# Performance work log

Hardware: AMD Instinct MI355X
Metric: run time of the kernel (lower is better)

The kernel has to match this reference:

```python
import math
import jax, jax.numpy as jnp
import numpy as np

C = 64
GRID = 2

def _conv1x1(x, W, b):
    # 1x1 conv == channel-mixing matmul: [B,C,H,W] x [O,C] -> [B,O,H,W]
    return jnp.einsum('bchw,oc->bohw', x, W) + b[None, :, None, None]

def setup_inputs() -> dict:
    key = jax.random.key(0)
    ks = jax.random.split(key, 11)
    s = 1.0 / math.sqrt(C)
    def w(k):
        return jax.random.normal(k, (C, C), dtype=jnp.float32) * s
    def bias(k):
        return jax.random.normal(k, (C,), dtype=jnp.float32) * 0.02
    return {
        'x': jax.random.normal(ks[0], (2, C, 128, 128), dtype=jnp.float32),
        'Wq': w(ks[1]), 'bq': bias(ks[2]),
        'Wk': w(ks[3]), 'bk': bias(ks[4]),
        'Wa': w(ks[5]), 'ba': bias(ks[6]),
        'Wb': w(ks[7]), 'bb': bias(ks[8]),
        'Wo': w(ks[9]), 'bo': bias(ks[10]),
    }

def reference(x, Wq, bq, Wk, bk, Wa, ba, Wb, bb, Wo, bo):
    B, c, H, W = x.shape
    g = GRID
    rh, rw = H // g, W // g  # H,W chosen divisible by grid -> no reflect pad
    N = rh * rw
    R = g * g

    q = _conv1x1(x, Wq, bq)
    k = _conv1x1(x, Wk, bk)
    a = _conv1x1(x, Wa, ba)
    bt = _conv1x1(x, Wb, bb)

    def regionize(t):
        # [B,C,H,W] -> [B, R, C, N] with N = rh*rw row-major per region
        return t.reshape(B, c, g, rh, g, rw).transpose(0, 2, 4, 1, 3, 5).reshape(B, R, c, N)

    qr, kr, ar, br = regionize(q), regionize(k), regionize(a), regionize(bt)

    # attn[b,r,n,m] = softmax_m( q^T k / sqrt(C) )
    attn = jax.nn.softmax(jnp.einsum('brcn,brcm->brnm', qr, kr) / math.sqrt(c), axis=-1)

    # out_r = alpha @ attn + beta @ attn^T
    out = (jnp.einsum('brcj,brjm->brcm', ar, attn)
           + jnp.einsum('brcj,brmj->brcm', br, attn))

    # [B,R,C,N] -> [B,C,H,W]
    out = out.reshape(B, g, g, c, rh, rw).transpose(0, 3, 1, 4, 2, 5).reshape(B, c, H, W)
    return _conv1x1(out, Wo, bo)
```

## Files before the change

kernel.cpp:

```cpp
#include <hip/hip_runtime.h>


typedef __attribute__((ext_vector_type(8)))  short bf16x8;
typedef __attribute__((ext_vector_type(16))) float f32x16;

#define MFMA32(a, b, c) __builtin_amdgcn_mfma_f32_32x32x16_bf16(a, b, c, 0, 0, 0)

constexpr int REG_ELEMS = 4096 * 64;
constexpr size_t QP_OFF    = 0;
constexpr size_t KP_OFF    = 4u  << 20;
constexpr size_t ATL_OFF   = 8u  << 20;
constexpr size_t BTL_OFF   = 12u << 20;
constexpr size_t OUTP_OFF  = 16u << 20;
constexpr size_t LNV_OFF   = 20u << 20;
constexpr size_t LPART_OFF = (20u << 20) + (128u << 10);

constexpr float QSCALE = 0.18033688011112042f;

__device__ __forceinline__ short f2bf(float f) {
    union { float f; unsigned u; } v; v.f = f;
    unsigned r = v.u + 0x7fffu + ((v.u >> 16) & 1u);
    return (short)(r >> 16);
}
__device__ __forceinline__ float bf2f(short s) {
    union { unsigned u; float f; } v; v.u = ((unsigned)(unsigned short)s) << 16;
    return v.f;
}
__device__ __forceinline__ unsigned fbits(float f) {
    union { float f; unsigned u; } v; v.f = f; return v.u;
}
__device__ __forceinline__ unsigned pack_trunc(float e0, float e1) {
    return __builtin_amdgcn_perm(fbits(e1), fbits(e0), 0x07060302u);
}
__device__ __forceinline__ f32x16 zero16() {
    f32x16 z;
    #pragma unroll
    for (int i = 0; i < 16; ++i) z[i] = 0.f;
    return z;
}
__device__ __forceinline__ float fexp2(float x) {
#if __has_builtin(__builtin_amdgcn_exp2f)
    return __builtin_amdgcn_exp2f(x);
#else
    return exp2f(x);
#endif
}
__device__ __forceinline__ void permswap32(unsigned& a, unsigned& b, bool hi) {
#if __has_builtin(__builtin_amdgcn_permlane32_swap)
    auto r = __builtin_amdgcn_permlane32_swap(a, b, false, false);
    a = r[0]; b = r[1];
#elif __has_builtin(__builtin_amdgcn_permlane32_swap_b32)
    auto r = __builtin_amdgcn_permlane32_swap_b32(a, b, false, false);
    a = r[0]; b = r[1];
#else
    unsigned ax = (unsigned)__shfl_xor((int)a, 32);
    unsigned bx = (unsigned)__shfl_xor((int)b, 32);
    unsigned na = hi ? bx : a;
    unsigned nb = hi ? b  : ax;
    a = na; b = nb;
#endif
}

typedef __attribute__((address_space(1))) const unsigned char as1_t;
typedef __attribute__((address_space(3))) unsigned char as3_t;
__device__ __forceinline__ void stage16(const void* g, void* l) {
    __builtin_amdgcn_global_load_lds((as1_t*)g, (as3_t*)l, 16, 0, 0);
}

__global__ __launch_bounds__(256) void k_conv_in(
    const float* __restrict__ x,
    const float* __restrict__ Wq, const float* __restrict__ bq,
    const float* __restrict__ Wk, const float* __restrict__ bk,
    const float* __restrict__ Wa, const float* __restrict__ ba,
    const float* __restrict__ Wb, const float* __restrict__ bb,
    char* __restrict__ ws)
{
    const int tid  = threadIdx.x;
    const int blk  = blockIdx.x;
    const int wseg = blk & 1;
    const int h    = (blk >> 1) & 127;
    const int b    = blk >> 8;
    const int br   = b * 4 + (h >> 6) * 2 + wseg;
    const int n0   = (h & 63) * 64;

    __shared__ float xs[64][68];
    __shared__ short trans[2][64][72];

    const float* xp = x + ((size_t)b * 64 * 16384) + (size_t)h * 128 + wseg * 64;
    #pragma unroll
    for (int r = 0; r < 4; ++r) {
        int idx = r * 256 + tid;
        int c   = idx >> 4;
        int w4  = (idx & 15) << 2;
        *(float4*)&xs[c][w4] = *(const float4*)(xp + (size_t)c * 16384 + w4);
    }
    __syncthreads();

    const int lane = tid & 63;
    const int wid  = tid >> 6;
    const int col  = lane & 31;
    const int l5   = lane >> 5;
    const int pH   = wid & 1;
    const int oH   = wid >> 1;
    const int px   = pH * 32 + col;
    const int oc   = oH * 32 + col;

    bf16x8 xhi[4], xlo[4];
    #pragma unroll
    for (int s = 0; s < 4; ++s) {
        union { bf16x8 v; short sh[8]; } uh, ul;
        #pragma unroll
        for (int e = 0; e < 8; ++e) {
            float xv = xs[s * 16 + l5 * 8 + e][px];
            short hh = f2bf(xv);
            uh.sh[e] = hh;
            ul.sh[e] = f2bf(xv - bf2f(hh));
        }
        xhi[s] = uh.v; xlo[s] = ul.v;
    }

    #pragma unroll
    for (int mat = 0; mat < 4; ++mat) {
        const float* Wsel = (mat == 0) ? Wq : (mat == 1) ? Wk : (mat == 2) ? Wa : Wb;
        const float* bsel = (mat == 0) ? bq : (mat == 1) ? bk : (mat == 2) ? ba : bb;

        bf16x8 whi[4], wlo[4];
        const float* wrow = Wsel + (size_t)oc * 64;
        #pragma unroll
        for (int s = 0; s < 4; ++s) {
            float4 f0 = *(const float4*)(wrow + s * 16 + l5 * 8);
            float4 f1 = *(const float4*)(wrow + s * 16 + l5 * 8 + 4);
            float wf[8] = { f0.x, f0.y, f0.z, f0.w, f1.x, f1.y, f1.z, f1.w };
            union { bf16x8 v; short sh[8]; } uh, ul;
            #pragma unroll
            for (int e = 0; e < 8; ++e) {
                short hh = f2bf(wf[e]);
                uh.sh[e] = hh;
                ul.sh[e] = f2bf(wf[e] - bf2f(hh));
            }
            whi[s] = uh.v; wlo[s] = ul.v;
        }

        f32x16 d = zero16();
        #pragma unroll
        for (int s = 0; s < 4; ++s) {
            d = MFMA32(xhi[s], whi[s], d);
            d = MFMA32(xhi[s], wlo[s], d);
            d = MFMA32(xlo[s], whi[s], d);
        }

        const float bias = bsel[oc];
        if (mat < 2) {
            const float sc = (mat == 0) ? QSCALE : 1.0f;
            #pragma unroll
            for (int r = 0; r < 16; ++r) {
                int pxl = pH * 32 + (r & 3) + 8 * (r >> 2) + 4 * l5;
                trans[mat][pxl][oc] = f2bf((d[r] + bias) * sc);
            }
        } else {
            short* base = (short*)(ws + (mat == 2 ? ATL_OFF : BTL_OFF))
                          + (size_t)br * REG_ELEMS;
            const int sw   = (oc >> 1) & 3;
            const int tile = (n0 >> 5) + pH;
            #pragma unroll
            for (int q = 0; q < 4; ++q) {
                short tmp4[4];
                #pragma unroll
                for (int rr = 0; rr < 4; ++rr) tmp4[rr] = f2bf(d[4 * q + rr] + bias);
                int segp = q ^ sw;
                short* p = base + (size_t)tile * 2048 + oc * 32 + segp * 8 + 4 * l5;
                *(uint2*)p = *(uint2*)tmp4;
            }
        }
    }
    __syncthreads();

    #pragma unroll
    for (int rep = 0; rep < 4; ++rep) {
        int idx  = rep * 256 + tid;
        int mat2 = idx >> 9;
        int row  = (idx >> 3) & 63;
        int seg  = idx & 7;
        short* dst = (short*)(ws + (mat2 ? KP_OFF : QP_OFF))
                     + (size_t)br * REG_ELEMS + (size_t)(n0 + row) * 64
                     + (seg ^ (row & 7)) * 8;
        *(uint4*)dst = *(uint4*)&trans[mat2][row][seg * 8];
    }
}

__global__ __launch_bounds__(256, 2) void k_stats(char* __restrict__ ws)
{
    const int tid  = threadIdx.x;
    const int br   = blockIdx.x & 7;
    const int nt   = (blockIdx.x >> 3) & 63;
    const int ms   = blockIdx.x >> 9;
    const int lane = tid & 63;
    const int w    = tid >> 6;
    const int wn   = w & 1;
    const int wi   = w >> 1;
    const int col  = lane & 31;
    const int l5   = lane >> 5;

    const short* Qb  = (const short*)(ws + QP_OFF) + (size_t)br * REG_ELEMS;
    const char*  Kbb = ws + KP_OFF + (size_t)br * REG_ELEMS * 2
                       + (size_t)ms * 262144;

    __shared__ __align__(16) char smem[16896];

    const int nrow = nt * 64 + wn * 32 + col;
    bf16x8 afr[4];
    #pragma unroll
    for (int s = 0; s < 4; ++s)
        afr[s] = *(const bf16x8*)(Qb + (size_t)nrow * 64 + (((2*s+l5) ^ (col & 7)) * 8));

    float sm[16];
    #pragma unroll
    for (int r = 0; r < 16; ++r) sm[r] = 0.f;

    {
        const char* g = Kbb + (size_t)w * 2048 + lane * 16;
        char* l = smem + w * 2048;
        stage16(g, l); stage16(g + 1024, l + 1024);
    }

    #pragma unroll 2
    for (int slab = 0; slab < 32; ++slab) {
        __syncthreads();
        if (slab + 1 < 32) {
            const char* g = Kbb + (size_t)(slab + 1) * 8192 + w * 2048 + lane * 16;
            char* l = smem + ((slab + 1) & 1) * 8192 + w * 2048;
            stage16(g, l); stage16(g + 1024, l + 1024);
        }
        const short* Ks = (const short*)(smem + (slab & 1) * 8192);
        f32x16 d = zero16();
        #pragma unroll
        for (int s = 0; s < 4; ++s) {
            bf16x8 bf = *(const bf16x8*)(Ks + (wi * 32 + col) * 64
                                         + ((2*s+l5) ^ (col & 7)) * 8);
            d = MFMA32(afr[s], bf, d);
        }
        #pragma unroll
        for (int r = 0; r < 16; ++r) sm[r] += fexp2(d[r]);
    }

    #pragma unroll
    for (int off = 1; off < 32; off <<= 1)
        #pragma unroll
        for (int r = 0; r < 16; ++r) sm[r] += __shfl_xor(sm[r], off);

    __syncthreads();
    float* Lred = (float*)(smem + 16384);
    if (col == 0) {
        #pragma unroll
        for (int r = 0; r < 16; ++r)
            Lred[w * 32 + ((r & 3) + 8 * (r >> 2) + 4 * l5)] = sm[r];
    }
    __syncthreads();
    if (tid < 64) {
        int wn2 = tid >> 5, nl = tid & 31;
        float L = Lred[wn2 * 32 + nl] + Lred[(wn2 + 2) * 32 + nl];
        ((float*)(ws + LPART_OFF))[(size_t)ms * 32768 + (size_t)br * 4096
                                   + nt * 64 + tid] = L;
    }
}

__global__ __launch_bounds__(256) void k_ascale(char* __restrict__ ws)
{
    const int tid = threadIdx.x;
    const int br  = blockIdx.x & 7;
    const int nt  = blockIdx.x >> 3;

    __shared__ float Larr[64];

    if (tid < 64) {
        const float* Lp = (const float*)(ws + LPART_OFF);
        const size_t idx = (size_t)br * 4096 + nt * 64 + tid;
        float li = 1.0f / (Lp[idx] + Lp[32768 + idx]);
        Larr[tid] = li;
        ((float*)(ws + LNV_OFF))[idx] = li;
    }
    __syncthreads();

    short* Ab = (short*)(ws + ATL_OFF) + (size_t)br * REG_ELEMS + (size_t)nt * 4096;
    #pragma unroll
    for (int rep = 0; rep < 2; ++rep) {
        int id = rep * 256 + tid;
        int t = id >> 8, c = (id >> 2) & 63, s = id & 3;
        int sg = s ^ ((c >> 1) & 3);
        int jl = t * 32 + sg * 8;
        short* p = Ab + (size_t)t * 2048 + c * 32 + s * 8;
        uint4 v = *(uint4*)p;
        short* sp = (short*)&v;
        short o[8];
        #pragma unroll
        for (int e = 0; e < 8; ++e) o[e] = f2bf(bf2f(sp[e]) * Larr[jl + e]);
        *(uint4*)p = *(uint4*)o;
    }
}

__global__ __launch_bounds__(256, 2) void k_attn(char* __restrict__ ws)
{
    const int tid  = threadIdx.x;
    const int br   = blockIdx.x & 7;
    const int mt   = blockIdx.x >> 3;
    const int lane = tid & 63;
    const int w    = tid >> 6;
    const int wm   = w & 1;
    const int wj   = w >> 1;
    const int col  = lane & 31;
    const int l5   = lane >> 5;
    const bool hi  = (l5 != 0);

    const char* Qbb = ws + QP_OFF  + (size_t)br * REG_ELEMS * 2;
    const char* Kbb = ws + KP_OFF  + (size_t)br * REG_ELEMS * 2;
    const char* Abb = ws + ATL_OFF + (size_t)br * REG_ELEMS * 2;
    const char* Bbb = ws + BTL_OFF + (size_t)br * REG_ELEMS * 2;
    const float* Lnv = (const float*)(ws + LNV_OFF) + (size_t)br * 4096;
    short* OutPb    = (short*)(ws + OUTP_OFF) + (size_t)br * REG_ELEMS;

    __shared__ __align__(16) char smem[32768];

    const int mrow = mt * 64 + wm * 32 + col;
    const short* msrc = (const short*)(wj == 0 ? Kbb : Qbb) + (size_t)mrow * 64;
    bf16x8 mf[4];
    #pragma unroll
    for (int s = 0; s < 4; ++s)
        mf[s] = *(const bf16x8*)(msrc + ((2*s+l5) ^ (col & 7)) * 8);

    f32x16 accL = zero16(), accH = zero16();

    const char* gsb = (w == 0) ? Qbb : (w == 1) ? Kbb : (w == 2) ? Abb : Bbb;

    {
        const char* g = gsb + lane * 16;
        char* l = smem + w * 4096 + lane * 16;
        #pragma unroll
        for (int i = 0; i < 4; ++i) stage16(g + i * 1024, l + i * 1024);
    }

    #pragma unroll 2
    for (int slab = 0; slab < 128; ++slab) {
        __syncthreads();
        if (slab + 1 < 128) {
            const char* g = gsb + (size_t)(slab + 1) * 4096 + lane * 16;
            char* l = smem + ((slab + 1) & 1) * 16384 + w * 4096 + lane * 16;
            #pragma unroll
            for (int i = 0; i < 4; ++i) stage16(g + i * 1024, l + i * 1024);
        }
        const char* sb = smem + (slab & 1) * 16384;
        const short* js = (const short*)(sb + (wj == 0 ? 0 : 4096));
        const short* ts = (const short*)(sb + (wj == 0 ? 8192 : 12288));

        f32x16 d = zero16();
        #pragma unroll
        for (int s = 0; s < 4; ++s) {
            bf16x8 a = *(const bf16x8*)(js + col * 64 + ((2*s+l5) ^ (col & 7)) * 8);
            d = MFMA32(a, mf[s], d);
        }

        unsigned Wp[8];
        #pragma unroll
        for (int q = 0; q < 4; ++q) {
            Wp[2*q]   = pack_trunc(fexp2(d[4*q]),   fexp2(d[4*q+1]));
            Wp[2*q+1] = pack_trunc(fexp2(d[4*q+2]), fexp2(d[4*q+3]));
        }

        #pragma unroll
        for (int k16 = 0; k16 < 2; ++k16) {
            unsigned u0 = Wp[4*k16+0], u1 = Wp[4*k16+1];
            unsigned u2 = Wp[4*k16+2], u3 = Wp[4*k16+3];
            permswap32(u0, u2, hi);
            permswap32(u1, u3, hi);
            union { uint4 u; bf16x8 v; } fr;
            fr.u.x = u0; fr.u.y = u1; fr.u.z = u2; fr.u.w = u3;

            const int swz = ((2*k16 + l5) ^ ((col >> 1) & 3)) * 8;
            bf16x8 bL = *(const bf16x8*)(ts + col * 32 + swz);
            bf16x8 bH = *(const bf16x8*)(ts + (col + 32) * 32 + swz);
            accL = MFMA32(fr.v, bL, accL);
            accH = MFMA32(fr.v, bH, accH);
        }
    }

    __syncthreads();
    float* red = (float*)smem;
    if (wj == 0) {
        #pragma unroll
        for (int r = 0; r < 16; ++r) {
            int ml = wm * 32 + (r & 3) + 8 * (r >> 2) + 4 * l5;
            red[ml * 68 + col]      = accL[r];
            red[ml * 68 + 32 + col] = accH[r];
        }
    }
    __syncthreads();
    if (wj == 1) {
        #pragma unroll
        for (int r = 0; r < 16; ++r) {
            int ml = wm * 32 + (r & 3) + 8 * (r >> 2) + 4 * l5;
            float li = Lnv[mt * 64 + ml];
            red[ml * 68 + col]      += li * accL[r];
            red[ml * 68 + 32 + col] += li * accH[r];
        }
    }
    __syncthreads();
    {
        const int m  = tid >> 2;
        const int c0 = (tid & 3) * 16;
        const float* rp = red + m * 68 + c0;
        uint4 p0, p1;
        p0.x = pack_trunc(rp[0],  rp[1]);  p0.y = pack_trunc(rp[2],  rp[3]);
        p0.z = pack_trunc(rp[4],  rp[5]);  p0.w = pack_trunc(rp[6],  rp[7]);
        p1.x = pack_trunc(rp[8],  rp[9]);  p1.y = pack_trunc(rp[10], rp[11]);
        p1.z = pack_trunc(rp[12], rp[13]); p1.w = pack_trunc(rp[14], rp[15]);
        short* orow = OutPb + (size_t)(mt * 64 + m) * 64 + c0;
        *(uint4*)orow       = p0;
        *(uint4*)(orow + 8) = p1;
    }
}

__global__ __launch_bounds__(256) void k_conv_out(
    const char* __restrict__ ws,
    const float* __restrict__ Wo, const float* __restrict__ bo,
    float* __restrict__ out)
{
    const int tid  = threadIdx.x;
    const int lane = tid & 63;
    const int sub  = tid >> 6;
    const int blk  = blockIdx.x;
    const int br   = blk & 7;
    const int nt   = (blk >> 3) * 4 + sub;
    const int col  = lane & 31;
    const int l5   = lane >> 5;

    const short* OutPb = (const short*)(ws + OUTP_OFF) + (size_t)br * REG_ELEMS;

    bf16x8 afr[4];
    const short* arow = OutPb + (size_t)(nt * 32 + col) * 64 + l5 * 8;
    #pragma unroll
    for (int s = 0; s < 4; ++s) afr[s] = *(const bf16x8*)(arow + s * 16);

    bf16x8 bw[2][4];
    #pragma unroll
    for (int oh = 0; oh < 2; ++oh) {
        const float* wrow = Wo + (size_t)(oh * 32 + col) * 64 + l5 * 8;
        #pragma unroll
        for (int s = 0; s < 4; ++s) {
            float4 f0 = *(const float4*)(wrow + s * 16);
            float4 f1 = *(const float4*)(wrow + s * 16 + 4);
            union { bf16x8 v; short sh[8]; } u;
            u.sh[0] = f2bf(f0.x); u.sh[1] = f2bf(f0.y);
            u.sh[2] = f2bf(f0.z); u.sh[3] = f2bf(f0.w);
            u.sh[4] = f2bf(f1.x); u.sh[5] = f2bf(f1.y);
            u.sh[6] = f2bf(f1.z); u.sh[7] = f2bf(f1.w);
            bw[oh][s] = u.v;
        }
    }

    f32x16 d0 = zero16(), d1 = zero16();
    #pragma unroll
    for (int s = 0; s < 4; ++s) {
        d0 = MFMA32(afr[s], bw[0][s], d0);
        d1 = MFMA32(afr[s], bw[1][s], d1);
    }

    const int b  = br >> 2;
    const int gi = (br >> 1) & 1;
    const int gj = br & 1;

    #pragma unroll
    for (int oh = 0; oh < 2; ++oh) {
        const int oc = oh * 32 + col;
        const float bias = bo[oc];
        const f32x16& d = oh ? d1 : d0;
        #pragma unroll
        for (int q = 0; q < 4; ++q) {
            int nloc = 8 * q + 4 * l5;
            int nreg = nt * 32 + nloc;
            int wp   = nreg & 63;
            int ip   = nreg >> 6;
            float4 v = make_float4(d[4*q+0] + bias, d[4*q+1] + bias,
                                   d[4*q+2] + bias, d[4*q+3] + bias);
            float* op = out + ((size_t)(b * 64 + oc)) * 16384
                        + (size_t)(gi * 64 + ip) * 128 + gj * 64 + wp;
            *(float4*)op = v;
        }
    }
}

extern "C" void kernel_launch(void* const* d_in, const int* in_sizes, int n_in,
                              void* d_out, int out_size, void* d_ws, size_t ws_size,
                              hipStream_t stream)
{
    const float* x  = (const float*)d_in[0];
    const float* Wq = (const float*)d_in[1];
    const float* bq = (const float*)d_in[2];
    const float* Wk = (const float*)d_in[3];
    const float* bk = (const float*)d_in[4];
    const float* Wa = (const float*)d_in[5];
    const float* ba = (const float*)d_in[6];
    const float* Wb = (const float*)d_in[7];
    const float* bb = (const float*)d_in[8];
    const float* Wo = (const float*)d_in[9];
    const float* bo = (const float*)d_in[10];
    char* ws   = (char*)d_ws;
    float* out = (float*)d_out;

    hipLaunchKernelGGL(k_conv_in,  dim3(512),  dim3(256), 0, stream,
                       x, Wq, bq, Wk, bk, Wa, ba, Wb, bb, ws);
    hipLaunchKernelGGL(k_stats,    dim3(1024), dim3(256), 0, stream, ws);
    hipLaunchKernelGGL(k_ascale,   dim3(512),  dim3(256), 0, stream, ws);
    hipLaunchKernelGGL(k_attn,     dim3(512),  dim3(256), 0, stream, ws);
    hipLaunchKernelGGL(k_conv_out, dim3(256),  dim3(256), 0, stream,
                       ws, Wo, bo, out);
}
```

Before: 205.2 us.

## Split j-range across warp pairs and give each warp both m-halves in attention kernel

```diff
diff --git a/kernel.cpp b/kernel.cpp
--- a/kernel.cpp
+++ b/kernel.cpp
@@ -305,8 +305,8 @@
     const int mt   = blockIdx.x >> 3;
     const int lane = tid & 63;
     const int w    = tid >> 6;
-    const int wm   = w & 1;
-    const int wj   = w >> 1;
+    const int wj   = w & 1;
+    const int jsw  = w >> 1;
     const int col  = lane & 31;
     const int l5   = lane >> 5;
     const bool hi  = (l5 != 0);
@@ -318,89 +318,144 @@
     const float* Lnv = (const float*)(ws + LNV_OFF) + (size_t)br * 4096;
     short* OutPb    = (short*)(ws + OUTP_OFF) + (size_t)br * REG_ELEMS;
 
-    __shared__ __align__(16) char smem[32768];
-
-    const int mrow = mt * 64 + wm * 32 + col;
-    const short* msrc = (const short*)(wj == 0 ? Kbb : Qbb) + (size_t)mrow * 64;
-    bf16x8 mf[4];
-    #pragma unroll
-    for (int s = 0; s < 4; ++s)
-        mf[s] = *(const bf16x8*)(msrc + ((2*s+l5) ^ (col & 7)) * 8);
-
-    f32x16 accL = zero16(), accH = zero16();
+    __shared__ __align__(16) char smem[65536];
+
+    const short* msrcb = (const short*)(wj == 0 ? Kbb : Qbb);
+    bf16x8 mf[2][4];
+    #pragma unroll
+    for (int h = 0; h < 2; ++h) {
+        const short* mr = msrcb + (size_t)(mt * 64 + h * 32 + col) * 64;
+        #pragma unroll
+        for (int s = 0; s < 4; ++s)
+            mf[h][s] = *(const bf16x8*)(mr + ((2*s+l5) ^ (col & 7)) * 8);
+    }
+
+    f32x16 acc00 = zero16(), acc01 = zero16();
+    f32x16 acc10 = zero16(), acc11 = zero16();
 
     const char* gsb = (w == 0) ? Qbb : (w == 1) ? Kbb : (w == 2) ? Abb : Bbb;
 
     {
-        const char* g = gsb + lane * 16;
-        char* l = smem + w * 4096 + lane * 16;
-        #pragma unroll
-        for (int i = 0; i < 4; ++i) stage16(g + i * 1024, l + i * 1024);
+        #pragma unroll
+        for (int h = 0; h < 2; ++h) {
+            const char* g = gsb + (size_t)h * 262144 + lane * 16;
+            char* l = smem + h * 16384 + w * 4096 + lane * 16;
+            #pragma unroll
+            for (int i = 0; i < 4; ++i) stage16(g + i * 1024, l + i * 1024);
+        }
     }
 
     #pragma unroll 2
-    for (int slab = 0; slab < 128; ++slab) {
+    for (int rnd = 0; rnd < 64; ++rnd) {
         __syncthreads();
-        if (slab + 1 < 128) {
-            const char* g = gsb + (size_t)(slab + 1) * 4096 + lane * 16;
-            char* l = smem + ((slab + 1) & 1) * 16384 + w * 4096 + lane * 16;
-            #pragma unroll
-            for (int i = 0; i < 4; ++i) stage16(g + i * 1024, l + i * 1024);
-        }
-        const char* sb = smem + (slab & 1) * 16384;
-        const short* js = (const short*)(sb + (wj == 0 ? 0 : 4096));
+        if (rnd + 1 < 64) {
+            #pragma unroll
+            for (int h = 0; h < 2; ++h) {
+                const char* g = gsb + (size_t)h * 262144
+                                + (size_t)(rnd + 1) * 4096 + lane * 16;
+                char* l = smem + ((rnd + 1) & 1) * 32768 + h * 16384
+                          + w * 4096 + lane * 16;
+                #pragma unroll
+                for (int i = 0; i < 4; ++i) stage16(g + i * 1024, l + i * 1024);
+            }
+        }
+        const char* sb = smem + (rnd & 1) * 32768 + jsw * 16384;
+        const short* jr = (const short*)(sb + (wj == 0 ? 0 : 4096));
         const short* ts = (const short*)(sb + (wj == 0 ? 8192 : 12288));
 
-        f32x16 d = zero16();
+        bf16x8 a[4];
+        #pragma unroll
+        for (int s = 0; s < 4; ++s)
+            a[s] = *(const bf16x8*)(jr + col * 64 + ((2*s+l5) ^ (col & 7)) * 8);
+
+        f32x16 d0 = zero16(), d1 = zero16();
         #pragma unroll
         for (int s = 0; s < 4; ++s) {
-            bf16x8 a = *(const bf16x8*)(js + col * 64 + ((2*s+l5) ^ (col & 7)) * 8);
-            d = MFMA32(a, mf[s], d);
-        }
-
-        unsigned Wp[8];
+            d0 = MFMA32(a[s], mf[0][s], d0);
+            d1 = MFMA32(a[s], mf[1][s], d1);
+        }
+
+        unsigned W0[8], W1[8];
         #pragma unroll
         for (int q = 0; q < 4; ++q) {
-            Wp[2*q]   = pack_trunc(fexp2(d[4*q]),   fexp2(d[4*q+1]));
-            Wp[2*q+1] = pack_trunc(fexp2(d[4*q+2]), fexp2(d[4*q+3]));
+            W0[2*q]   = pack_trunc(fexp2(d0[4*q]),   fexp2(d0[4*q+1]));
+            W0[2*q+1] = pack_trunc(fexp2(d0[4*q+2]), fexp2(d0[4*q+3]));
+            W1[2*q]   = pack_trunc(fexp2(d1[4*q]),   fexp2(d1[4*q+1]));
+            W1[2*q+1] = pack_trunc(fexp2(d1[4*q+2]), fexp2(d1[4*q+3]));
         }
 
         #pragma unroll
         for (int k16 = 0; k16 < 2; ++k16) {
-            unsigned u0 = Wp[4*k16+0], u1 = Wp[4*k16+1];
-            unsigned u2 = Wp[4*k16+2], u3 = Wp[4*k16+3];
+            unsigned u0 = W0[4*k16+0], u1 = W0[4*k16+1];
+            unsigned u2 = W0[4*k16+2], u3 = W0[4*k16+3];
             permswap32(u0, u2, hi);
             permswap32(u1, u3, hi);
-            union { uint4 u; bf16x8 v; } fr;
-            fr.u.x = u0; fr.u.y = u1; fr.u.z = u2; fr.u.w = u3;
+            union { uint4 u; bf16x8 v; } fr0;
+            fr0.u.x = u0; fr0.u.y = u1; fr0.u.z = u2; fr0.u.w = u3;
+
+            unsigned v0 = W1[4*k16+0], v1 = W1[4*k16+1];
+            unsigned v2 = W1[4*k16+2], v3 = W1[4*k16+3];
+            permswap32(v0, v2, hi);
+            permswap32(v1, v3, hi);
+            union { uint4 u; bf16x8 v; } fr1;
+            fr1.u.x = v0; fr1.u.y = v1; fr1.u.z = v2; fr1.u.w = v3;
 
             const int swz = ((2*k16 + l5) ^ ((col >> 1) & 3)) * 8;
             bf16x8 bL = *(const bf16x8*)(ts + col * 32 + swz);
             bf16x8 bH = *(const bf16x8*)(ts + (col + 32) * 32 + swz);
-            accL = MFMA32(fr.v, bL, accL);
-            accH = MFMA32(fr.v, bH, accH);
+            acc00 = MFMA32(fr0.v, bL, acc00);
+            acc01 = MFMA32(fr0.v, bH, acc01);
+            acc10 = MFMA32(fr1.v, bL, acc10);
+            acc11 = MFMA32(fr1.v, bH, acc11);
         }
     }
 
     __syncthreads();
     float* red = (float*)smem;
-    if (wj == 0) {
-        #pragma unroll
-        for (int r = 0; r < 16; ++r) {
-            int ml = wm * 32 + (r & 3) + 8 * (r >> 2) + 4 * l5;
-            red[ml * 68 + col]      = accL[r];
-            red[ml * 68 + 32 + col] = accH[r];
-        }
-    }
-    __syncthreads();
-    if (wj == 1) {
-        #pragma unroll
-        for (int r = 0; r < 16; ++r) {
-            int ml = wm * 32 + (r & 3) + 8 * (r >> 2) + 4 * l5;
-            float li = Lnv[mt * 64 + ml];
-            red[ml * 68 + col]      += li * accL[r];
-            red[ml * 68 + 32 + col] += li * accH[r];
-        }
+    if (w == 0) {
+        #pragma unroll
+        for (int h = 0; h < 2; ++h)
+            #pragma unroll
+            for (int r = 0; r < 16; ++r) {
+                int ml = h * 32 + (r & 3) + 8 * (r >> 2) + 4 * l5;
+                red[ml * 68 + col]      = h ? acc10[r] : acc00[r];
+                red[ml * 68 + 32 + col] = h ? acc11[r] : acc01[r];
+            }
+    }
+    __syncthreads();
+    if (w == 2) {
+        #pragma unroll
+        for (int h = 0; h < 2; ++h)
+            #pragma unroll
+            for (int r = 0; r < 16; ++r) {
+                int ml = h * 32 + (r & 3) + 8 * (r >> 2) + 4 * l5;
+                red[ml * 68 + col]      += h ? acc10[r] : acc00[r];
+                red[ml * 68 + 32 + col] += h ? acc11[r] : acc01[r];
+            }
+    }
+    __syncthreads();
+    if (w == 1) {
+        #pragma unroll
+        for (int h = 0; h < 2; ++h)
+            #pragma unroll
+            for (int r = 0; r < 16; ++r) {
+                int ml = h * 32 + (r & 3) + 8 * (r >> 2) + 4 * l5;
+                float li = Lnv[mt * 64 + ml];
+                red[ml * 68 + col]      += li * (h ? acc10[r] : acc00[r]);
+                red[ml * 68 + 32 + col] += li * (h ? acc11[r] : acc01[r]);
+            }
+    }
+    __syncthreads();
+    if (w == 3) {
+        #pragma unroll
+        for (int h = 0; h < 2; ++h)
+            #pragma unroll
+            for (int r = 0; r < 16; ++r) {
+                int ml = h * 32 + (r & 3) + 8 * (r >> 2) + 4 * l5;
+                float li = Lnv[mt * 64 + ml];
+                red[ml * 68 + col]      += li * (h ? acc10[r] : acc00[r]);
+                red[ml * 68 + 32 + col] += li * (h ? acc11[r] : acc01[r]);
+            }
     }
     __syncthreads();
     {
```

After: 202.2 us (median of 2 runs). About the same (-1.4%).
